# Kernel optimization log

Measured on AMD Instinct MI355X. Metric: run time of the kernel, lower is better.

The kernel has to match this reference:

```python
import jax, jax.numpy as jnp
import numpy as np

D_IN = 1024
D_OUT = 1024


def setup_inputs() -> dict:
    key = jax.random.key(0)
    kx, kq, kk, kv = jax.random.split(key, 4)
    x = jax.random.normal(kx, (4, 2048, D_IN), dtype=jnp.float32)
    s = 1.0 / np.sqrt(D_IN)
    Wq = jax.random.normal(kq, (D_IN, D_OUT), dtype=jnp.float32) * s
    Wk = jax.random.normal(kk, (D_IN, D_OUT), dtype=jnp.float32) * s
    Wv = jax.random.normal(kv, (D_IN, D_OUT), dtype=jnp.float32) * s
    return {"x": x, "Wq": Wq, "Wk": Wk, "Wv": Wv}


def reference(x, Wq, Wk, Wv):
    # x: [B, S, d_in]; W*: [d_in, d_out]
    B, S, _ = x.shape
    q = x @ Wq  # [B, S, d_out]
    k = x @ Wk
    v = x @ Wv
    scale = 1.0 / jnp.sqrt(jnp.asarray(k.shape[-1], x.dtype))
    scores = jnp.einsum("bqd,bkd->bqk", q, k) * scale  # [B, S, S]
    # causal mask: positions j > i masked to -inf (triu, diagonal=1)
    causal = jnp.tril(jnp.ones((S, S), dtype=bool))
    scores = jnp.where(causal[None, :, :], scores, -jnp.inf)
    attn = jax.nn.softmax(scores, axis=-1)  # dropout p=0.0 -> identity
    return jnp.einsum("bqk,bkd->bqd", attn, v)
```

## Files before the change

kernel.cpp:

```cpp
#include <hip/hip_runtime.h>
#include <hip/hip_bf16.h>

#define NB 4
#define SB 2048
#define DD 1024
#define BM 128
#define BN 128
#define BK 32

typedef __attribute__((ext_vector_type(8))) short bf16x8;
typedef __attribute__((ext_vector_type(4))) short bf16x4;
typedef __attribute__((ext_vector_type(4))) float f32x4;
typedef unsigned int u32;

__device__ __forceinline__ float bf2f(unsigned short u) {
    return __uint_as_float(((u32)u) << 16);
}
__device__ __forceinline__ short f2bf(float f) {
    u32 u = __float_as_uint(f);
    u32 r = (u + 0x7fffu + ((u >> 16) & 1u)) >> 16;
    return (short)r;
}

__device__ __forceinline__ void wait_vm12() {
    asm volatile("s_waitcnt vmcnt(12)" ::: "memory");
}
__device__ __forceinline__ void wait_vm6() {
    asm volatile("s_waitcnt vmcnt(6)" ::: "memory");
}
__device__ __forceinline__ void wait_vm0() {
    asm volatile("s_waitcnt vmcnt(0)" ::: "memory");
}
__device__ __forceinline__ void barrier_raw() {
    __builtin_amdgcn_s_barrier();
    asm volatile("" ::: "memory");
}

__device__ __forceinline__ void mfma_step(const short* As, const short* Bs,
                                          f32x4 (&acc)[4][4], int lane, int wave)
{
    const int wm = (wave >> 1) * 64, wn = (wave & 1) * 64;
    const int fr = lane & 15;
    const int quad = lane >> 4;
    bf16x8 af[4], bf[4];
#pragma unroll
    for (int t = 0; t < 4; t++) {
        af[t] = *(const bf16x8*)&As[(wm + t * 16 + fr) * BK + quad * 8];
        bf[t] = *(const bf16x8*)&Bs[(wn + t * 16 + fr) * BK + quad * 8];
    }
#pragma unroll
    for (int mt = 0; mt < 4; mt++)
#pragma unroll
        for (int nt = 0; nt < 4; nt++)
            acc[mt][nt] = __builtin_amdgcn_mfma_f32_16x16x32_bf16(
                af[mt], bf[nt], acc[mt][nt], 0, 0, 0);
}

__device__ __forceinline__ void mfma_step_swz(const short* As, const short* Bs,
                                              f32x4 (&acc)[4][4], int lane,
                                              int wave)
{
    const int wm = (wave >> 1) * 64, wn = (wave & 1) * 64;
    const int fr = lane & 15;
    const int qa = (lane >> 4) ^ ((fr >> 1) & 3);
    bf16x8 af[4], bf[4];
#pragma unroll
    for (int t = 0; t < 4; t++) {
        af[t] = *(const bf16x8*)&As[(wm + t * 16 + fr) * BK + qa * 8];
        bf[t] = *(const bf16x8*)&Bs[(wn + t * 16 + fr) * BK + qa * 8];
    }
#pragma unroll
    for (int mt = 0; mt < 4; mt++)
#pragma unroll
        for (int nt = 0; nt < 4; nt++)
            acc[mt][nt] = __builtin_amdgcn_mfma_f32_16x16x32_bf16(
                af[mt], bf[nt], acc[mt][nt], 0, 0, 0);
}

__device__ __forceinline__ void mfma_step_pv_swz(const short* As,
                                                 const short* Bs,
                                                 f32x4 (&acc)[2][4], int lane,
                                                 int wave)
{
    const int wm = wave * 32;
    const int fr = lane & 15;
    const int qa = (lane >> 4) ^ ((fr >> 1) & 3);
    bf16x8 af[2], bf[4];
#pragma unroll
    for (int t = 0; t < 2; t++)
        af[t] = *(const bf16x8*)&As[(wm + t * 16 + fr) * BK + qa * 8];
#pragma unroll
    for (int t = 0; t < 4; t++)
        bf[t] = *(const bf16x8*)&Bs[(t * 16 + fr) * BK + qa * 8];
#pragma unroll
    for (int mt = 0; mt < 2; mt++)
#pragma unroll
        for (int nt = 0; nt < 4; nt++)
            acc[mt][nt] = __builtin_amdgcn_mfma_f32_16x16x32_bf16(
                af[mt], bf[nt], acc[mt][nt], 0, 0, 0);
}

__device__ __forceinline__ void stage128x32(const short* __restrict__ g, int ld,
                                            short* lds, int tid) {
    const int wave = tid >> 6, lane = tid & 63;
    const int r = lane >> 2;
    const int c = ((lane & 3) ^ ((lane >> 3) & 3)) * 8;
#pragma unroll
    for (int i = 0; i < 2; i++) {
        const int chunk = wave * 2 + i;
        const short* gp = g + (size_t)(chunk * 16 + r) * ld + c;
        __builtin_amdgcn_global_load_lds(
            (const __attribute__((address_space(1))) u32*)gp,
            (__attribute__((address_space(3))) u32*)(lds + chunk * 512 + lane * 8),
            16, 0, 0);
    }
}

__device__ __forceinline__ void stage64x32(const short* __restrict__ g, int ld,
                                           short* lds, int tid) {
    const int wave = tid >> 6, lane = tid & 63;
    const int r = lane >> 2;
    const int c = ((lane & 3) ^ ((lane >> 3) & 3)) * 8;
    const short* gp = g + (size_t)(wave * 16 + r) * ld + c;
    __builtin_amdgcn_global_load_lds(
        (const __attribute__((address_space(1))) u32*)gp,
        (__attribute__((address_space(3))) u32*)(lds + wave * 512 + lane * 8),
        16, 0, 0);
}

__device__ __forceinline__ void stage_tile256(const short* __restrict__ gA,
                                              int lda,
                                              const short* __restrict__ gB,
                                              int ldb, short* slot, int tid) {
    const int w = tid >> 6, l = tid & 63;
    const int lr = l >> 2;
    const int lc = ((l & 3) ^ ((l >> 3) & 3)) * 8;
#pragma unroll
    for (int i = 0; i < 4; i++) {
        const int ks = i >> 1;
        const int row = (i & 1) * 128 + w * 16 + lr;
        const short* gp = gA + (size_t)row * lda + ks * 32 + lc;
        __builtin_amdgcn_global_load_lds(
            (const __attribute__((address_space(1))) u32*)gp,
            (__attribute__((address_space(3))) u32*)(slot + i * 4096 + w * 512 + l * 8),
            16, 0, 0);
    }
    short* bbase = slot + 16384;
#pragma unroll
    for (int i = 0; i < 2; i++) {
        const int row = w * 16 + lr;
        const short* gp = gB + (size_t)row * ldb + i * 32 + lc;
        __builtin_amdgcn_global_load_lds(
            (const __attribute__((address_space(1))) u32*)gp,
            (__attribute__((address_space(3))) u32*)(bbase + i * 4096 + w * 512 + l * 8),
            16, 0, 0);
    }
}

__device__ __forceinline__ void stage_f32_128x32(const float* __restrict__ g,
                                                 int ld, short* lds, int tid) {
    const int r = tid >> 1;
    const int c = (tid & 1) * 16;
    const float* gp = &g[(size_t)r * ld + c];
    float4 v0 = *(const float4*)(gp + 0);
    float4 v1 = *(const float4*)(gp + 4);
    float4 v2 = *(const float4*)(gp + 8);
    float4 v3 = *(const float4*)(gp + 12);
    bf16x8 o0, o1;
    o0[0] = f2bf(v0.x); o0[1] = f2bf(v0.y); o0[2] = f2bf(v0.z); o0[3] = f2bf(v0.w);
    o0[4] = f2bf(v1.x); o0[5] = f2bf(v1.y); o0[6] = f2bf(v1.z); o0[7] = f2bf(v1.w);
    o1[0] = f2bf(v2.x); o1[1] = f2bf(v2.y); o1[2] = f2bf(v2.z); o1[3] = f2bf(v2.w);
    o1[4] = f2bf(v3.x); o1[5] = f2bf(v3.y); o1[6] = f2bf(v3.z); o1[7] = f2bf(v3.w);
    *(bf16x8*)&lds[r * BK + c] = o0;
    *(bf16x8*)&lds[r * BK + c + 8] = o1;
}

__global__ __launch_bounds__(256) void prep_mm(
    const float* __restrict__ x, const float* __restrict__ Wq,
    const float* __restrict__ Wk, const float* __restrict__ Wv,
    short* __restrict__ xb, short* __restrict__ Wvt, float* __restrict__ Mp4)
{
    __shared__ short As[BM * BK], Bs[BN * BK];
    __shared__ short t[64][65];
    const int bx = blockIdx.x;
    const int tid = threadIdx.x;
    if (bx < 256) {
        const int ch = bx >> 6;
        const int t64 = bx & 63;
        const int m0 = (t64 >> 3) * BM;
        const int n0 = (t64 & 7) * BN;
        const int kbase = ch * 256;
        const int lane = tid & 63, wave = tid >> 6;
        f32x4 acc[4][4];
#pragma unroll
        for (int a = 0; a < 4; a++)
#pragma unroll
            for (int b = 0; b < 4; b++) acc[a][b] = (f32x4){0.f, 0.f, 0.f, 0.f};
        for (int k0 = 0; k0 < 256; k0 += BK) {
            stage_f32_128x32(Wk + (size_t)m0 * DD + kbase + k0, DD, As, tid);
            stage_f32_128x32(Wq + (size_t)n0 * DD + kbase + k0, DD, Bs, tid);
            __syncthreads();
            mfma_step(As, Bs, acc, lane, wave);
            __syncthreads();
        }
        const int wm = (wave >> 1) * 64, wn = (wave & 1) * 64;
        const int fr = lane & 15, quad = lane >> 4;
        float* Mc = Mp4 + (size_t)ch * DD * DD;
#pragma unroll
        for (int mt = 0; mt < 4; mt++)
#pragma unroll
            for (int nt = 0; nt < 4; nt++)
#pragma unroll
                for (int r = 0; r < 4; r++) {
                    const size_t m = m0 + wm + mt * 16 + quad * 4 + r;
                    const size_t n = n0 + wn + nt * 16 + fr;
                    Mc[m * DD + n] = acc[mt][nt][r];
                }
        return;
    }
    if (bx < 4352) {
        const size_t i = ((size_t)(bx - 256) * 256 + tid) * 8;
        float4 a = *(const float4*)&x[i];
        float4 b = *(const float4*)&x[i + 4];
        bf16x8 o;
        o[0] = f2bf(a.x); o[1] = f2bf(a.y); o[2] = f2bf(a.z); o[3] = f2bf(a.w);
        o[4] = f2bf(b.x); o[5] = f2bf(b.y); o[6] = f2bf(b.z); o[7] = f2bf(b.w);
        *(bf16x8*)&xb[i] = o;
        return;
    }
    const int rr = bx - 4352;
    const int k0 = (rr & 15) * 64;
    const int n0 = (rr >> 4) * 64;
    {
        const int r = tid >> 4;
        const int c = (tid & 15) * 4;
#pragma unroll
        for (int i = 0; i < 4; i++) {
            float4 v = *(const float4*)&Wv[(size_t)(k0 + i * 16 + r) * DD + n0 + c];
            t[i * 16 + r][c + 0] = f2bf(v.x);
            t[i * 16 + r][c + 1] = f2bf(v.y);
            t[i * 16 + r][c + 2] = f2bf(v.z);
            t[i * 16 + r][c + 3] = f2bf(v.w);
        }
    }
    __syncthreads();
    {
        const int r = tid >> 3;
        const int c = (tid & 7) * 8;
#pragma unroll
        for (int i = 0; i < 2; i++) {
            bf16x8 o;
#pragma unroll
            for (int j = 0; j < 8; j++) o[j] = t[c + j][i * 32 + r];
            *(bf16x8*)&Wvt[(size_t)(n0 + i * 32 + r) * DD + k0 + c] = o;
        }
    }
}

__global__ __launch_bounds__(256) void mm_reduce(const float* __restrict__ Mp4,
                                                 short* __restrict__ Mp)
{
    const size_t e = ((size_t)blockIdx.x * 256 + threadIdx.x) * 4;
    const size_t N = (size_t)DD * DD;
    float4 s = *(const float4*)&Mp4[e];
#pragma unroll
    for (int c = 1; c < 4; c++) {
        float4 p = *(const float4*)&Mp4[c * N + e];
        s.x += p.x; s.y += p.y; s.z += p.z; s.w += p.w;
    }
    bf16x4 o;
    o[0] = f2bf(s.x); o[1] = f2bf(s.y); o[2] = f2bf(s.z); o[3] = f2bf(s.w);
    *(bf16x4*)&Mp[e] = o;
}

__global__ __launch_bounds__(512) void tv_gemm(
    const short* __restrict__ xb, const short* __restrict__ Mp,
    const short* __restrict__ Wvt, short* __restrict__ T,
    short* __restrict__ Vt)
{
    __shared__ short lds[3 * 24576];
    const int lin = blockIdx.x + 8 * blockIdx.y;
    const int swz = (lin & 7) * 32 + (lin >> 3);
    const int n0 = (swz & 7) * 128;
    const int m0 = (swz >> 3) * 256;
    const int isv = blockIdx.z;
    const short* Bt = isv ? Wvt : Mp;
    const short* Ap = xb + (size_t)m0 * DD;
    const short* Bp = Bt + (size_t)n0 * DD;
    const int tid = threadIdx.x;
    const int lane = tid & 63, wave = tid >> 6;
    f32x4 acc[4][4];
#pragma unroll
    for (int a = 0; a < 4; a++)
#pragma unroll
        for (int b = 0; b < 4; b++) acc[a][b] = (f32x4){0.f, 0.f, 0.f, 0.f};

    stage_tile256(Ap, DD, Bp, DD, lds, tid);
    stage_tile256(Ap + 64, DD, Bp + 64, DD, lds + 24576, tid);
    for (int j = 0; j < 16; ++j) {
        if (j < 14)
            stage_tile256(Ap + (j + 2) * 64, DD, Bp + (j + 2) * 64, DD,
                          lds + ((j + 2) % 3) * 24576, tid);
        if (j < 14)       wait_vm12();
        else if (j == 14) wait_vm6();
        else              wait_vm0();
        barrier_raw();
        short* slot = lds + (j % 3) * 24576;
        __builtin_amdgcn_s_setprio(1);
        mfma_step_swz(slot, slot + 16384, acc, lane, wave);
        mfma_step_swz(slot + 8192, slot + 16384 + 4096, acc, lane, wave);
        __builtin_amdgcn_s_setprio(0);
        barrier_raw();
    }

    const int wm = (wave >> 1) * 64, wn = (wave & 1) * 64;
    const int fr = lane & 15, quad = lane >> 4;
    if (!isv) {
#pragma unroll
        for (int mt = 0; mt < 4; mt++)
#pragma unroll
            for (int nt = 0; nt < 4; nt++)
#pragma unroll
                for (int r = 0; r < 4; r++) {
                    const size_t m = m0 + wm + mt * 16 + quad * 4 + r;
                    const size_t n = n0 + wn + nt * 16 + fr;
                    T[m * DD + n] = f2bf(acc[mt][nt][r]);
                }
    } else {
        const int bb = m0 >> 11;
        const int s0 = (m0 & (SB - 1)) + wm + quad * 4;
        short* Vb = Vt + (size_t)bb * DD * SB;
#pragma unroll
        for (int mt = 0; mt < 4; mt++)
#pragma unroll
            for (int nt = 0; nt < 4; nt++) {
                const size_t n = n0 + wn + nt * 16 + fr;
                const size_t s = s0 + mt * 16;
                bf16x4 o;
#pragma unroll
                for (int r = 0; r < 4; r++) o[r] = f2bf(acc[mt][nt][r]);
                *(bf16x4*)&Vb[n * SB + s] = o;
            }
    }
}

__global__ __launch_bounds__(256) void scores_mfma(
    const short* __restrict__ T, const short* __restrict__ xb,
    short* __restrict__ Sc)
{
    const int bx = blockIdx.x;
    const int idx = (bx & 7) * 34 + (bx >> 3);
    int qt = (int)((__fsqrt_rn(4.f * idx + 1.f) - 1.f) * 0.5f);
    while ((qt + 1) * (qt + 2) <= idx) qt++;
    while (qt * (qt + 1) > idx) qt--;
    const int kt = idx - qt * (qt + 1);
    const int qm0 = qt * BM;
    const int kn0 = kt * 64;
    const int b = blockIdx.y;
    __shared__ short As[2 * BM * BK], Bs[2 * 64 * BK];
    const short* Tq = T + (size_t)b * SB * DD + (size_t)qm0 * DD;
    const short* Xk = xb + (size_t)b * SB * DD + (size_t)kn0 * DD;
    short* Sb = Sc + (size_t)b * SB * SB;
    const int tid = threadIdx.x;
    const int lane = tid & 63, wave = tid >> 6;
    f32x4 acc[2][4];
#pragma unroll
    for (int a = 0; a < 2; a++)
#pragma unroll
        for (int c = 0; c < 4; c++) acc[a][c] = (f32x4){0.f, 0.f, 0.f, 0.f};
    for (int k0 = 0; k0 < DD; k0 += 2 * BK) {
        stage128x32(Tq + k0, DD, As, tid);
        stage128x32(Tq + k0 + BK, DD, As + BM * BK, tid);
        stage64x32(Xk + k0, DD, Bs, tid);
        stage64x32(Xk + k0 + BK, DD, Bs + 64 * BK, tid);
        __syncthreads();
        mfma_step_pv_swz(As, Bs, acc, lane, wave);
        mfma_step_pv_swz(As + BM * BK, Bs + 64 * BK, acc, lane, wave);
        __syncthreads();
    }
    const int fr = lane & 15, quad = lane >> 4;
    const float scale = 0.03125f;
#pragma unroll
    for (int mt = 0; mt < 2; mt++)
#pragma unroll
        for (int nt = 0; nt < 4; nt++)
#pragma unroll
            for (int r = 0; r < 4; r++) {
                const size_t q = qm0 + wave * 32 + mt * 16 + quad * 4 + r;
                const size_t k = kn0 + nt * 16 + fr;
                Sb[q * SB + k] = f2bf(acc[mt][nt][r] * scale);
            }
}

__global__ __launch_bounds__(256) void softmax_kernel(short* __restrict__ Sc)
{
    const int row = blockIdx.x;
    const int i = row & (SB - 1);
    const int jlim = ((i >> 7) + 1) << 7;
    short* r = Sc + (size_t)row * SB;
    const int t = threadIdx.x;
    const int lane = t & 63, wave = t >> 6;
    __shared__ float red[8];

    const int j0 = t * 8;
    bf16x8 in = {0, 0, 0, 0, 0, 0, 0, 0};
    if (j0 <= i) in = *(const bf16x8*)&r[j0];
    float v[8];
    float mx = -1e30f;
#pragma unroll
    for (int e = 0; e < 8; e++) {
        const float s = (j0 + e <= i) ? bf2f((unsigned short)in[e]) : -1e30f;
        v[e] = s;
        mx = fmaxf(mx, s);
    }
#pragma unroll
    for (int o = 32; o > 0; o >>= 1) mx = fmaxf(mx, __shfl_down(mx, o));
    if (lane == 0) red[wave] = mx;
    __syncthreads();
    mx = fmaxf(fmaxf(red[0], red[1]), fmaxf(red[2], red[3]));

    float sum = 0.f;
#pragma unroll
    for (int e = 0; e < 8; e++) {
        const float x = (j0 + e <= i) ? __expf(v[e] - mx) : 0.f;
        v[e] = x;
        sum += x;
    }
#pragma unroll
    for (int o = 32; o > 0; o >>= 1) sum += __shfl_down(sum, o);
    if (lane == 0) red[4 + wave] = sum;
    __syncthreads();
    const float inv = 1.0f / (red[4] + red[5] + red[6] + red[7]);
    if (j0 < jlim) {
        bf16x8 o;
#pragma unroll
        for (int e = 0; e < 8; e++) o[e] = f2bf(v[e] * inv);
        *(bf16x8*)&r[j0] = o;
    }
}

__global__ __launch_bounds__(256) void pv_mfma(
    const short* __restrict__ P, const short* __restrict__ Vt,
    float* __restrict__ O)
{
    __shared__ short As[4 * BM * BK];
    __shared__ short Bs[4 * 64 * BK];
    const int n0 = blockIdx.x * 64;
    const int pair = blockIdx.y;
    const int b = blockIdx.z;
    const short* Pb = P + (size_t)b * SB * SB;
    const short* Vb = Vt + (size_t)b * DD * SB;
    float* Ob = O + (size_t)b * SB * DD;
    const int tid = threadIdx.x;
    const int lane = tid & 63, wave = tid >> 6;
    const int fr = lane & 15, quad = lane >> 4;
    for (int half = 0; half < 2; ++half) {
        const int qt = half ? (15 - pair) : pair;
        const int qm0 = qt * BM;
        const int nj = (qt + 1) * 2;
        const short* Pq = Pb + (size_t)qm0 * SB;
        const short* Vn = Vb + (size_t)n0 * SB;
        f32x4 acc[2][4];
#pragma unroll
        for (int a = 0; a < 2; a++)
#pragma unroll
            for (int c = 0; c < 4; c++) acc[a][c] = (f32x4){0.f, 0.f, 0.f, 0.f};
        stage128x32(Pq, SB, As, tid);
        stage128x32(Pq + BK, SB, As + BM * BK, tid);
        stage64x32(Vn, SB, Bs, tid);
        stage64x32(Vn + BK, SB, Bs + 64 * BK, tid);
        for (int j = 0; j < nj; ++j) {
            const int cur = j & 1;
            const short* as = As + cur * (2 * BM * BK);
            const short* bs = Bs + cur * (2 * 64 * BK);
            if (j + 1 < nj) {
                const int off = (j + 1) * 64;
                short* an = As + (cur ^ 1) * (2 * BM * BK);
                short* bn = Bs + (cur ^ 1) * (2 * 64 * BK);
                stage128x32(Pq + off, SB, an, tid);
                stage128x32(Pq + off + BK, SB, an + BM * BK, tid);
                stage64x32(Vn + off, SB, bn, tid);
                stage64x32(Vn + off + BK, SB, bn + 64 * BK, tid);
                wait_vm6();
            } else {
                wait_vm0();
            }
            barrier_raw();
            mfma_step_pv_swz(as, bs, acc, lane, wave);
            mfma_step_pv_swz(as + BM * BK, bs + 64 * BK, acc, lane, wave);
            barrier_raw();
        }
#pragma unroll
        for (int mt = 0; mt < 2; mt++)
#pragma unroll
            for (int nt = 0; nt < 4; nt++)
#pragma unroll
                for (int r = 0; r < 4; r++) {
                    const size_t q = qm0 + wave * 32 + mt * 16 + quad * 4 + r;
                    const size_t n = n0 + nt * 16 + fr;
                    Ob[q * DD + n] = acc[mt][nt][r];
                }
    }
}

extern "C" void kernel_launch(void* const* d_in, const int* in_sizes, int n_in,
                              void* d_out, int out_size, void* d_ws, size_t ws_size,
                              hipStream_t stream)
{
    const float* x  = (const float*)d_in[0];
    const float* Wq = (const float*)d_in[1];
    const float* Wk = (const float*)d_in[2];
    const float* Wv = (const float*)d_in[3];
    float* out = (float*)d_out;

    const size_t XE = (size_t)NB * SB * DD;
    const size_t WE = (size_t)DD * DD;
    short* xb  = (short*)d_ws;
    short* T   = xb + XE;
    short* Vt  = T + XE;
    short* Sc  = Vt + XE;
    float* Pp  = (float*)(Sc + (size_t)NB * SB * SB);
    short* Wvt = (short*)(Pp + (size_t)NB * 1024 * DD);
    short* Mp  = Wvt + WE;
    float* Mp4 = (float*)Sc;

    prep_mm<<<dim3(256 + 4096 + 256), 256, 0, stream>>>(
        x, Wq, Wk, Wv, xb, Wvt, Mp4);
    mm_reduce<<<dim3(1024), 256, 0, stream>>>(Mp4, Mp);
    tv_gemm<<<dim3(8, 32, 2), 512, 0, stream>>>(xb, Mp, Wvt, T, Vt);
    scores_mfma<<<dim3(272, NB), 256, 0, stream>>>(T, xb, Sc);
    softmax_kernel<<<dim3(NB * SB), 256, 0, stream>>>(Sc);
    pv_mfma<<<dim3(DD / 64, 8, NB), 256, 0, stream>>>(Sc, Vt, out);
}
```

Baseline: 226.7 us.

## Enlarge tv_gemm tiles to 256x256 with double-buffered LDS pipeline

The T/V projection GEMM now computes 256x256 output tiles per block instead of 256x128, with each of the 8 waves owning a 128x64 sub-tile (8x4 MFMA accumulators). The three-slot LDS ring is replaced by two buffers of 64 KB total, and the wait count is adjusted to match. Larger tiles raise arithmetic intensity and halve B-tile reloads, but they double the accumulator registers, which lowers occupancy. The grid also shrinks to 256 blocks, and the prefetch distance drops from two stages to one.

```diff
diff --git a/kernel.cpp b/kernel.cpp
--- a/kernel.cpp
+++ b/kernel.cpp
@@ -22,8 +22,8 @@
     return (short)r;
 }
 
-__device__ __forceinline__ void wait_vm12() {
-    asm volatile("s_waitcnt vmcnt(12)" ::: "memory");
+__device__ __forceinline__ void wait_vm8() {
+    asm volatile("s_waitcnt vmcnt(8)" ::: "memory");
 }
 __device__ __forceinline__ void wait_vm6() {
     asm volatile("s_waitcnt vmcnt(6)" ::: "memory");
@@ -56,27 +56,6 @@
                 af[mt], bf[nt], acc[mt][nt], 0, 0, 0);
 }
 
-__device__ __forceinline__ void mfma_step_swz(const short* As, const short* Bs,
-                                              f32x4 (&acc)[4][4], int lane,
-                                              int wave)
-{
-    const int wm = (wave >> 1) * 64, wn = (wave & 1) * 64;
-    const int fr = lane & 15;
-    const int qa = (lane >> 4) ^ ((fr >> 1) & 3);
-    bf16x8 af[4], bf[4];
-#pragma unroll
-    for (int t = 0; t < 4; t++) {
-        af[t] = *(const bf16x8*)&As[(wm + t * 16 + fr) * BK + qa * 8];
-        bf[t] = *(const bf16x8*)&Bs[(wn + t * 16 + fr) * BK + qa * 8];
-    }
-#pragma unroll
-    for (int mt = 0; mt < 4; mt++)
-#pragma unroll
-        for (int nt = 0; nt < 4; nt++)
-            acc[mt][nt] = __builtin_amdgcn_mfma_f32_16x16x32_bf16(
-                af[mt], bf[nt], acc[mt][nt], 0, 0, 0);
-}
-
 __device__ __forceinline__ void mfma_step_pv_swz(const short* As,
                                                  const short* Bs,
                                                  f32x4 (&acc)[2][4], int lane,
@@ -94,6 +73,30 @@
         bf[t] = *(const bf16x8*)&Bs[(t * 16 + fr) * BK + qa * 8];
 #pragma unroll
     for (int mt = 0; mt < 2; mt++)
+#pragma unroll
+        for (int nt = 0; nt < 4; nt++)
+            acc[mt][nt] = __builtin_amdgcn_mfma_f32_16x16x32_bf16(
+                af[mt], bf[nt], acc[mt][nt], 0, 0, 0);
+}
+
+__device__ __forceinline__ void mfma_step256_swz(const short* As,
+                                                 const short* Bs,
+                                                 f32x4 (&acc)[8][4], int lane,
+                                                 int wave)
+{
+    const int wm = (wave >> 2) * 128;
+    const int wn = (wave & 3) * 64;
+    const int fr = lane & 15;
+    const int qa = (lane >> 4) ^ ((fr >> 1) & 3);
+    bf16x8 af[8], bf[4];
+#pragma unroll
+    for (int t = 0; t < 8; t++)
+        af[t] = *(const bf16x8*)&As[(wm + t * 16 + fr) * BK + qa * 8];
+#pragma unroll
+    for (int t = 0; t < 4; t++)
+        bf[t] = *(const bf16x8*)&Bs[(wn + t * 16 + fr) * BK + qa * 8];
+#pragma unroll
+    for (int mt = 0; mt < 8; mt++)
 #pragma unroll
         for (int nt = 0; nt < 4; nt++)
             acc[mt][nt] = __builtin_amdgcn_mfma_f32_16x16x32_bf16(
@@ -128,10 +131,8 @@
         16, 0, 0);
 }
 
-__device__ __forceinline__ void stage_tile256(const short* __restrict__ gA,
-                                              int lda,
-                                              const short* __restrict__ gB,
-                                              int ldb, short* slot, int tid) {
+__device__ __forceinline__ void stage256x64(const short* __restrict__ g, int ld,
+                                            short* base, int tid) {
     const int w = tid >> 6, l = tid & 63;
     const int lr = l >> 2;
     const int lc = ((l & 3) ^ ((l >> 3) & 3)) * 8;
@@ -139,20 +140,10 @@
     for (int i = 0; i < 4; i++) {
         const int ks = i >> 1;
         const int row = (i & 1) * 128 + w * 16 + lr;
-        const short* gp = gA + (size_t)row * lda + ks * 32 + lc;
+        const short* gp = g + (size_t)row * ld + ks * 32 + lc;
         __builtin_amdgcn_global_load_lds(
             (const __attribute__((address_space(1))) u32*)gp,
-            (__attribute__((address_space(3))) u32*)(slot + i * 4096 + w * 512 + l * 8),
-            16, 0, 0);
-    }
-    short* bbase = slot + 16384;
-#pragma unroll
-    for (int i = 0; i < 2; i++) {
-        const int row = w * 16 + lr;
-        const short* gp = gB + (size_t)row * ldb + i * 32 + lc;
-        __builtin_amdgcn_global_load_lds(
-            (const __attribute__((address_space(1))) u32*)gp,
-            (__attribute__((address_space(3))) u32*)(bbase + i * 4096 + w * 512 + l * 8),
+            (__attribute__((address_space(3))) u32*)(base + i * 4096 + w * 512 + l * 8),
             16, 0, 0);
     }
 }
@@ -278,46 +269,49 @@
     const short* __restrict__ Wvt, short* __restrict__ T,
     short* __restrict__ Vt)
 {
-    __shared__ short lds[3 * 24576];
-    const int lin = blockIdx.x + 8 * blockIdx.y;
-    const int swz = (lin & 7) * 32 + (lin >> 3);
-    const int n0 = (swz & 7) * 128;
-    const int m0 = (swz >> 3) * 256;
+    __shared__ short lds[2 * 32768];
+    const int lin = blockIdx.x + 4 * blockIdx.y;
+    const int swz = (lin & 7) * 16 + (lin >> 3);
+    const int n0 = (swz & 3) * 256;
+    const int m0 = (swz >> 2) * 256;
     const int isv = blockIdx.z;
     const short* Bt = isv ? Wvt : Mp;
     const short* Ap = xb + (size_t)m0 * DD;
     const short* Bp = Bt + (size_t)n0 * DD;
     const int tid = threadIdx.x;
     const int lane = tid & 63, wave = tid >> 6;
-    f32x4 acc[4][4];
-#pragma unroll
-    for (int a = 0; a < 4; a++)
+    f32x4 acc[8][4];
+#pragma unroll
+    for (int a = 0; a < 8; a++)
 #pragma unroll
         for (int b = 0; b < 4; b++) acc[a][b] = (f32x4){0.f, 0.f, 0.f, 0.f};
 
-    stage_tile256(Ap, DD, Bp, DD, lds, tid);
-    stage_tile256(Ap + 64, DD, Bp + 64, DD, lds + 24576, tid);
+    stage256x64(Ap, DD, lds, tid);
+    stage256x64(Bp, DD, lds + 16384, tid);
     for (int j = 0; j < 16; ++j) {
-        if (j < 14)
-            stage_tile256(Ap + (j + 2) * 64, DD, Bp + (j + 2) * 64, DD,
-                          lds + ((j + 2) % 3) * 24576, tid);
-        if (j < 14)       wait_vm12();
-        else if (j == 14) wait_vm6();
-        else              wait_vm0();
+        const int cur = j & 1;
+        short* slot = lds + cur * 32768;
+        if (j < 15) {
+            short* nxt = lds + (cur ^ 1) * 32768;
+            stage256x64(Ap + (j + 1) * 64, DD, nxt, tid);
+            stage256x64(Bp + (j + 1) * 64, DD, nxt + 16384, tid);
+            wait_vm8();
+        } else {
+            wait_vm0();
+        }
         barrier_raw();
-        short* slot = lds + (j % 3) * 24576;
         __builtin_amdgcn_s_setprio(1);
-        mfma_step_swz(slot, slot + 16384, acc, lane, wave);
-        mfma_step_swz(slot + 8192, slot + 16384 + 4096, acc, lane, wave);
+        mfma_step256_swz(slot, slot + 16384, acc, lane, wave);
+        mfma_step256_swz(slot + 8192, slot + 16384 + 8192, acc, lane, wave);
         __builtin_amdgcn_s_setprio(0);
         barrier_raw();
     }
 
-    const int wm = (wave >> 1) * 64, wn = (wave & 1) * 64;
+    const int wm = (wave >> 2) * 128, wn = (wave & 3) * 64;
     const int fr = lane & 15, quad = lane >> 4;
     if (!isv) {
 #pragma unroll
-        for (int mt = 0; mt < 4; mt++)
+        for (int mt = 0; mt < 8; mt++)
 #pragma unroll
             for (int nt = 0; nt < 4; nt++)
 #pragma unroll
@@ -331,7 +325,7 @@
         const int s0 = (m0 & (SB - 1)) + wm + quad * 4;
         short* Vb = Vt + (size_t)bb * DD * SB;
 #pragma unroll
-        for (int mt = 0; mt < 4; mt++)
+        for (int mt = 0; mt < 8; mt++)
 #pragma unroll
             for (int nt = 0; nt < 4; nt++) {
                 const size_t n = n0 + wn + nt * 16 + fr;
@@ -527,7 +521,7 @@
     prep_mm<<<dim3(256 + 4096 + 256), 256, 0, stream>>>(
         x, Wq, Wk, Wv, xb, Wvt, Mp4);
     mm_reduce<<<dim3(1024), 256, 0, stream>>>(Mp4, Mp);
-    tv_gemm<<<dim3(8, 32, 2), 512, 0, stream>>>(xb, Mp, Wvt, T, Vt);
+    tv_gemm<<<dim3(4, 32, 2), 512, 0, stream>>>(xb, Mp, Wvt, T, Vt);
     scores_mfma<<<dim3(272, NB), 256, 0, stream>>>(T, xb, Sc);
     softmax_kernel<<<dim3(NB * SB), 256, 0, stream>>>(Sc);
     pv_mfma<<<dim3(DD / 64, 8, NB), 256, 0, stream>>>(Sc, Vt, out);
```

Result: no change. 222.6 us (-1.8%).
